# Kernel optimization log

Measured on AMD Instinct MI355X. Metric: run time of the kernel, lower is better.

Reference implementation:

```python
import jax, jax.numpy as jnp
import numpy as np

B, L, D = 2, 2048, 1024
H, E = 16, 64  # n_heads, per-head dim (E_q=E_k=E_v)
EPS = 1e-5


def _layernorm(x):
    # fresh nn.LayerNorm each forward: gamma=1, beta=0, eps=1e-5 (biased var)
    mu = jnp.mean(x, axis=-1, keepdims=True)
    var = jnp.mean(jnp.square(x - mu), axis=-1, keepdims=True)
    return (x - mu) * jax.lax.rsqrt(var + EPS)


def setup_inputs() -> dict:
    key = jax.random.key(0)
    ks = jax.random.split(key, 9)
    s_in = 1.0 / np.sqrt(D)
    s_ctx = 1.0 / np.sqrt(H * E)
    return {
        "query": jax.random.normal(ks[0], (B, L, D), jnp.float32),
        "key": jax.random.normal(ks[1], (B, L, D), jnp.float32),
        "value": jax.random.normal(ks[2], (B, L, D), jnp.float32),
        # torch nn.Linear weights are [out_features, in_features]
        "W_Q": jax.random.uniform(ks[3], (H * E, D), jnp.float32, -s_in, s_in),
        "W_K": jax.random.uniform(ks[4], (H * E, D), jnp.float32, -s_in, s_in),
        "W_V": jax.random.uniform(ks[5], (H * E, D), jnp.float32, -s_in, s_in),
        "W_O": jax.random.uniform(ks[6], (D, H * E), jnp.float32, -s_ctx, s_ctx),
        "fc_w": jax.random.uniform(ks[7], (D, D), jnp.float32, -s_in, s_in),
        "fc_b": jax.random.uniform(ks[8], (D,), jnp.float32, -s_in, s_in),
    }


def reference(query, key, value, W_Q, W_K, W_V, W_O, fc_w, fc_b):
    b = query.shape[0]
    # projections -> [B, H, L, E]
    q = (query @ W_Q.T).reshape(b, -1, H, E).transpose(0, 2, 1, 3)
    k = (key @ W_K.T).reshape(b, -1, H, E).transpose(0, 2, 1, 3)
    v = (value @ W_V.T).reshape(b, -1, H, E).transpose(0, 2, 1, 3)
    scores = jnp.einsum('bhqe,bhke->bhqk', q, k) / np.sqrt(E).astype(np.float32)
    A = jax.nn.softmax(scores, axis=-1)                 # [B,H,Lq,Lk]
    ctx = jnp.einsum('bhqk,bhke->bhqe', A, v)           # [B,H,L,E]
    ctx = ctx.transpose(0, 2, 1, 3).reshape(b, -1, H * E)
    attn_out = ctx @ W_O.T                               # dropout = identity (eval)
    x = _layernorm(attn_out + query)
    out = x @ fc_w.T + fc_b                              # dropout = identity (eval)
    out = _layernorm(x + out)
    return out
```

## Files before the change

kernel.cpp:

```cpp
#include <hip/hip_runtime.h>
#include <stdint.h>

typedef unsigned short u16;
typedef __bf16 bf16x8 __attribute__((ext_vector_type(8)));
typedef __bf16 bf16x4 __attribute__((ext_vector_type(4)));
typedef float f32x4 __attribute__((ext_vector_type(4)));

#define MFMA16(a,b,c) __builtin_amdgcn_mfma_f32_16x16x32_bf16((a),(b),(c),0,0,0)

__device__ __forceinline__ bf16x4 pack4(float a, float b, float c, float d){
  bf16x4 r; r[0]=(__bf16)a; r[1]=(__bf16)b; r[2]=(__bf16)c; r[3]=(__bf16)d; return r;
}

__device__ __forceinline__ void gl2lds16(const void* g, void* l){
  __builtin_amdgcn_global_load_lds(
      (const __attribute__((address_space(1))) unsigned int*)g,
      (__attribute__((address_space(3))) unsigned int*)l, 16, 0, 0);
}

__device__ __forceinline__ bf16x8 ldsfrag(const u16* base, int row, int gr){
  return *(const bf16x8*)(base + row * 64 + ((gr ^ (row & 7)) << 3));
}

template<int NB>
__device__ __forceinline__ void gemm_core(const u16* __restrict__ A,
                                          const u16* __restrict__ Bt,
                                          int N, int K, int mode,
                                          void* __restrict__ Cout,
                                          const float* __restrict__ bias,
                                          float oscale)
{
  __shared__ u16 Al[NB][128 * 64];
  __shared__ u16 Bl[NB][128 * 64];
  const int tid  = threadIdx.x;
  const int lane = tid & 63;
  const int w    = tid >> 6;
  const int wr   = w >> 1, wc = w & 1;
  const int l15  = lane & 15, g = lane >> 4;
  const int rowBase = blockIdx.y << 7;
  const int colBase = blockIdx.x << 7;

  const int srow = tid >> 3;
  const int swz  = ((tid & 7) ^ (srow & 7)) << 3;
  const u16* Ag = A  + (size_t)(rowBase + srow) * K + swz;
  const u16* Bg = Bt + (size_t)(colBase + srow) * K + swz;

  f32x4 acc[4][4];
#pragma unroll
  for (int m = 0; m < 4; ++m)
#pragma unroll
    for (int n = 0; n < 4; ++n) acc[m][n] = f32x4{0.f, 0.f, 0.f, 0.f};

  auto stage = [&](int buf, int k0) {
#pragma unroll
    for (int i = 0; i < 4; ++i) {
      gl2lds16(Ag + (size_t)(i * 32) * K + k0, Al[buf] + i * 2048 + w * 512);
      gl2lds16(Bg + (size_t)(i * 32) * K + k0, Bl[buf] + i * 2048 + w * 512);
    }
  };
  auto compute = [&](int buf) {
    __builtin_amdgcn_s_setprio(1);
#pragma unroll
    for (int kk = 0; kk < 2; ++kk) {
      bf16x8 af[4], bfr[4];
#pragma unroll
      for (int m = 0; m < 4; ++m) af[m]  = ldsfrag(Al[buf], wr * 64 + m * 16 + l15, kk * 4 + g);
#pragma unroll
      for (int n = 0; n < 4; ++n) bfr[n] = ldsfrag(Bl[buf], wc * 64 + n * 16 + l15, kk * 4 + g);
#pragma unroll
      for (int m = 0; m < 4; ++m)
#pragma unroll
        for (int n = 0; n < 4; ++n)
          acc[m][n] = MFMA16(af[m], bfr[n], acc[m][n]);
    }
    __builtin_amdgcn_s_setprio(0);
  };

  if (NB == 2) {
    stage(0, 0);
    __syncthreads();
    int cur = 0;
    for (int k0 = 0; k0 < K; k0 += 64) {
      if (k0 + 64 < K) stage(cur ^ 1, k0 + 64);
      compute(cur);
      __syncthreads();
      cur ^= 1;
    }
  } else {
    for (int k0 = 0; k0 < K; k0 += 64) {
      stage(0, k0);
      __syncthreads();
      compute(0);
      __syncthreads();
    }
  }

#pragma unroll
  for (int m = 0; m < 4; ++m) {
#pragma unroll
    for (int n = 0; n < 4; ++n) {
      const int row0 = rowBase + wr * 64 + m * 16 + g * 4;
      const int col  = colBase + wc * 64 + n * 16 + l15;
      if (mode == 1) {
        const int b = row0 >> 11, l = row0 & 2047;
        const int h = col >> 6,  e = col & 63;
        *(bf16x4*)((u16*)Cout + ((size_t)((((b << 4) + h) << 6) | e) << 11) + l) =
            pack4(acc[m][n][0], acc[m][n][1], acc[m][n][2], acc[m][n][3]);
      } else {
#pragma unroll
        for (int r = 0; r < 4; ++r) {
          const int row = row0 + r;
          const float v = acc[m][n][r];
          if (mode == 0) {
            *(__bf16*)((u16*)Cout + (size_t)row * N + col) = (__bf16)(v * oscale);
          } else if (mode == 2) {
            ((float*)Cout)[(size_t)row * N + col] = v;
          } else {
            ((float*)Cout)[(size_t)row * N + col] = v + bias[col];
          }
        }
      }
    }
  }
}

#define QSCALE 0.18033688011112042f

__global__ __launch_bounds__(256) void k_proj(
    const u16* __restrict__ qb, const u16* __restrict__ kb, const u16* __restrict__ vb,
    const u16* __restrict__ wq, const u16* __restrict__ wk, const u16* __restrict__ wv,
    u16* __restrict__ Qp, u16* __restrict__ Kp, u16* __restrict__ Vt)
{
  const int z = blockIdx.z;
  const u16* A = (z == 0) ? qb : (z == 1) ? kb : vb;
  const u16* B = (z == 0) ? wq : (z == 1) ? wk : wv;
  void* C = (z == 0) ? (void*)Qp : (z == 1) ? (void*)Kp : (void*)Vt;
  gemm_core<1>(A, B, 1024, 1024, (z == 2) ? 1 : 0, C, nullptr, (z == 0) ? QSCALE : 1.0f);
}

__global__ __launch_bounds__(256) void k_gemm_f32(const u16* __restrict__ A,
                                                  const u16* __restrict__ B,
                                                  float* __restrict__ C)
{ gemm_core<2>(A, B, 1024, 1024, 2, (void*)C, nullptr, 1.0f); }

__global__ __launch_bounds__(256) void k_gemm_f32_bias(const u16* __restrict__ A,
                                                       const u16* __restrict__ B,
                                                       float* __restrict__ C,
                                                       const float* __restrict__ bias)
{ gemm_core<2>(A, B, 1024, 1024, 3, (void*)C, bias, 1.0f); }

__global__ __launch_bounds__(256) void k_attn(const u16* __restrict__ Qp,
                                              const u16* __restrict__ Kp,
                                              const u16* __restrict__ Vt,
                                              u16* __restrict__ ctx)
{
  __shared__ u16 Klds[2][64 * 64];
  __shared__ u16 Vlds[2][64 * 64];
  __shared__ u16 Plds[4 * 16 * 64];

  const int tid = threadIdx.x, lane = tid & 63, w = tid >> 6;
  const int l15 = lane & 15, g = lane >> 4, l7 = l15 & 7;
  const int bh = blockIdx.y, b = bh >> 4, h = bh & 15;
  const int q0 = blockIdx.x << 6;

  const u16* Qr = Qp + (((size_t)((b << 11) + q0 + (w << 4) + l15)) << 10) + (h << 6) + (g << 3);
  const bf16x8 bq0 = *(const bf16x8*)(Qr);
  const bf16x8 bq1 = *(const bf16x8*)(Qr + 32);

  f32x4 o[4];
#pragma unroll
  for (int f = 0; f < 4; ++f) o[f] = f32x4{0.f, 0.f, 0.f, 0.f};
  float dsum = 0.f;

  const int srow = tid >> 3;
  const int swz  = ((tid & 7) ^ (srow & 7)) << 3;
  const u16* Kg = Kp + (((size_t)((b << 11) + srow)) << 10) + (h << 6) + swz;
  const u16* Vg = Vt + (((size_t)((bh << 6) + srow)) << 11) + swz;
  u16* Pw = Plds + (w << 10);

  auto stage = [&](int buf, int j0) {
#pragma unroll
    for (int i = 0; i < 2; ++i) {
      gl2lds16(Kg + ((size_t)(j0 + i * 32) << 10), Klds[buf] + i * 2048 + w * 512);
      gl2lds16(Vg + ((size_t)(i * 32) << 11) + j0, Vlds[buf] + i * 2048 + w * 512);
    }
  };

  stage(0, 0);
  __syncthreads();
  int cur = 0;

  for (int j0 = 0; j0 < 2048; j0 += 64) {
    if (j0 + 64 < 2048) stage(cur ^ 1, j0 + 64);

    f32x4 s[4];
#pragma unroll
    for (int f = 0; f < 4; ++f) s[f] = f32x4{0.f, 0.f, 0.f, 0.f};
    __builtin_amdgcn_s_setprio(1);
#pragma unroll
    for (int kk = 0; kk < 2; ++kk) {
      const bf16x8 bq = kk ? bq1 : bq0;
#pragma unroll
      for (int f = 0; f < 4; ++f)
        s[f] = MFMA16(ldsfrag(Klds[cur], f * 16 + l15, kk * 4 + g), bq, s[f]);
    }
    __builtin_amdgcn_s_setprio(0);

#pragma unroll
    for (int f = 0; f < 4; ++f) {
      const float e0 = __builtin_amdgcn_exp2f(s[f][0]);
      const float e1 = __builtin_amdgcn_exp2f(s[f][1]);
      const float e2 = __builtin_amdgcn_exp2f(s[f][2]);
      const float e3 = __builtin_amdgcn_exp2f(s[f][3]);
      dsum += (e0 + e1) + (e2 + e3);
      *(bf16x4*)(Pw + l15 * 64 + ((((2 * f) + (g >> 1)) ^ l7) << 3) + ((g & 1) << 2)) =
          pack4(e0, e1, e2, e3);
    }
    asm volatile("s_waitcnt lgkmcnt(0)" ::: "memory");
    __builtin_amdgcn_sched_barrier(0);

    __builtin_amdgcn_s_setprio(1);
#pragma unroll
    for (int kk = 0; kk < 2; ++kk) {
      const bf16x8 pb = *(const bf16x8*)(Pw + l15 * 64 + (((kk * 4 + g) ^ l7) << 3));
#pragma unroll
      for (int f = 0; f < 4; ++f)
        o[f] = MFMA16(ldsfrag(Vlds[cur], f * 16 + l15, kk * 4 + g), pb, o[f]);
    }
    __builtin_amdgcn_s_setprio(0);
    __syncthreads();
    cur ^= 1;
  }

  dsum += __shfl_xor(dsum, 16, 64);
  dsum += __shfl_xor(dsum, 32, 64);
  const float inv = 1.0f / dsum;
  const size_t rowoff = (((size_t)((b << 11) + q0 + (w << 4) + l15)) << 10) + (h << 6);
#pragma unroll
  for (int f = 0; f < 4; ++f)
    *(bf16x4*)(ctx + rowoff + f * 16 + (g << 2)) =
        pack4(o[f][0] * inv, o[f][1] * inv, o[f][2] * inv, o[f][3] * inv);
}

__global__ __launch_bounds__(256) void k_add_ln(const float* __restrict__ a,
                                                const float* __restrict__ res,
                                                float* __restrict__ xo,
                                                u16* __restrict__ xb)
{
  const int row = blockIdx.x, tid = threadIdx.x;
  const size_t base = (size_t)row << 10;
  float4 t = ((const float4*)(a + base))[tid];
  const float4 rr = ((const float4*)(res + base))[tid];
  t.x += rr.x; t.y += rr.y; t.z += rr.z; t.w += rr.w;
  float s = t.x + t.y + t.z + t.w;
  float q = t.x * t.x + t.y * t.y + t.z * t.z + t.w * t.w;
#pragma unroll
  for (int d = 1; d < 64; d <<= 1) {
    s += __shfl_xor(s, d, 64);
    q += __shfl_xor(q, d, 64);
  }
  __shared__ float ps[4], pq[4];
  const int w = tid >> 6;
  if ((tid & 63) == 0) { ps[w] = s; pq[w] = q; }
  __syncthreads();
  s = ps[0] + ps[1] + ps[2] + ps[3];
  q = pq[0] + pq[1] + pq[2] + pq[3];
  const float mean = s * (1.0f / 1024.0f);
  const float var  = q * (1.0f / 1024.0f) - mean * mean;
  const float inv  = rsqrtf(var + 1e-5f);
  float4 o;
  o.x = (t.x - mean) * inv; o.y = (t.y - mean) * inv;
  o.z = (t.z - mean) * inv; o.w = (t.w - mean) * inv;
  ((float4*)(xo + base))[tid] = o;
  if (xb) {
    ((bf16x4*)(xb + base))[tid] = pack4(o.x, o.y, o.z, o.w);
  }
}

__global__ __launch_bounds__(256) void k_cvt3(const float* __restrict__ q,
                                              const float* __restrict__ k,
                                              const float* __restrict__ v,
                                              u16* __restrict__ qo,
                                              u16* __restrict__ ko,
                                              u16* __restrict__ vo)
{
  const int z = blockIdx.y;
  const float* src = (z == 0) ? q : (z == 1) ? k : v;
  u16* dst = (z == 0) ? qo : (z == 1) ? ko : vo;
  const int i = blockIdx.x * 256 + threadIdx.x;
  const float4 t = ((const float4*)src)[i];
  ((bf16x4*)dst)[i] = pack4(t.x, t.y, t.z, t.w);
}

__global__ __launch_bounds__(256) void k_cvt5(const float* __restrict__ a0,
                                              const float* __restrict__ a1,
                                              const float* __restrict__ a2,
                                              const float* __restrict__ a3,
                                              const float* __restrict__ a4,
                                              u16* __restrict__ o0, u16* __restrict__ o1,
                                              u16* __restrict__ o2, u16* __restrict__ o3,
                                              u16* __restrict__ o4)
{
  const int z = blockIdx.y;
  const float* src = (z == 0) ? a0 : (z == 1) ? a1 : (z == 2) ? a2 : (z == 3) ? a3 : a4;
  u16* dst = (z == 0) ? o0 : (z == 1) ? o1 : (z == 2) ? o2 : (z == 3) ? o3 : o4;
  const int i = blockIdx.x * 256 + threadIdx.x;
  const float4 t = ((const float4*)src)[i];
  ((bf16x4*)dst)[i] = pack4(t.x, t.y, t.z, t.w);
}

extern "C" void kernel_launch(void* const* d_in, const int* in_sizes, int n_in,
                              void* d_out, int out_size, void* d_ws, size_t ws_size,
                              hipStream_t stream)
{
  (void)in_sizes; (void)n_in; (void)out_size; (void)ws_size;
  const float* query = (const float*)d_in[0];
  const float* key   = (const float*)d_in[1];
  const float* value = (const float*)d_in[2];
  const float* W_Q   = (const float*)d_in[3];
  const float* W_K   = (const float*)d_in[4];
  const float* W_V   = (const float*)d_in[5];
  const float* W_O   = (const float*)d_in[6];
  const float* fc_w  = (const float*)d_in[7];
  const float* fc_b  = (const float*)d_in[8];
  float* out = (float*)d_out;
  char* ws = (char*)d_ws;

  u16*   qb   = (u16*)(ws + 0);
  u16*   kb   = (u16*)(ws + 8388608);
  u16*   vb   = (u16*)(ws + 16777216);
  u16*   wq   = (u16*)(ws + 25165824);
  u16*   wk   = (u16*)(ws + 27262976);
  u16*   wv   = (u16*)(ws + 29360128);
  u16*   wo   = (u16*)(ws + 31457280);
  u16*   fw   = (u16*)(ws + 33554432);
  u16*   Qp   = (u16*)(ws + 35651584);
  u16*   Kp   = (u16*)(ws + 44040192);
  u16*   Vt   = (u16*)(ws + 52428800);
  u16*   ctx  = (u16*)(ws + 60817408);
  float* attn = (float*)(ws + 69206016);
  float* x    = (float*)(ws + 85983232);
  u16*   xb   = vb;
  float* y    = (float*)(ws + 0);

  k_cvt3<<<dim3(4096, 3), 256, 0, stream>>>(query, key, value, qb, kb, vb);
  k_cvt5<<<dim3(1024, 5), 256, 0, stream>>>(W_Q, W_K, W_V, W_O, fc_w, wq, wk, wv, wo, fw);
  k_proj<<<dim3(8, 32, 3), 256, 0, stream>>>(qb, kb, vb, wq, wk, wv, Qp, Kp, Vt);
  k_attn<<<dim3(32, 32), 256, 0, stream>>>(Qp, Kp, Vt, ctx);
  k_gemm_f32<<<dim3(8, 32), 256, 0, stream>>>(ctx, wo, attn);
  k_add_ln<<<dim3(4096), 256, 0, stream>>>(attn, query, x, xb);
  k_gemm_f32_bias<<<dim3(8, 32), 256, 0, stream>>>(xb, fw, y, fc_b);
  k_add_ln<<<dim3(4096), 256, 0, stream>>>(y, x, out, nullptr);
}
```

Baseline: 170.6 us.

## Keep K/V fragments in registers, bf16 intermediates, narrower GEMM tiles for O/FC

Attention no longer stages K and V through shared memory with barriers. Each wave loads its K/V MFMA fragments straight from global memory into registers and prefetches the next tile, and the kernel gets an occupancy hint. The output and FC GEMMs use 128x64 tiles for twice as many blocks and write bf16 instead of fp32. The LayerNorm kernels now read bf16 inputs and no longer write the fp32 residual, which reduces memory traffic. In exchange, each wave loads K/V redundantly from global memory, and keeping the residual in bf16 lowers precision.

```diff
diff --git a/kernel.cpp b/kernel.cpp
--- a/kernel.cpp
+++ b/kernel.cpp
@@ -22,7 +22,7 @@
   return *(const bf16x8*)(base + row * 64 + ((gr ^ (row & 7)) << 3));
 }
 
-template<int NB>
+template<int NB, int BN>
 __device__ __forceinline__ void gemm_core(const u16* __restrict__ A,
                                           const u16* __restrict__ Bt,
                                           int N, int K, int mode,
@@ -30,47 +30,49 @@
                                           const float* __restrict__ bias,
                                           float oscale)
 {
+  constexpr int NF = BN / 32;
   __shared__ u16 Al[NB][128 * 64];
-  __shared__ u16 Bl[NB][128 * 64];
+  __shared__ u16 Bl[NB][BN * 64];
   const int tid  = threadIdx.x;
   const int lane = tid & 63;
   const int w    = tid >> 6;
   const int wr   = w >> 1, wc = w & 1;
   const int l15  = lane & 15, g = lane >> 4;
   const int rowBase = blockIdx.y << 7;
-  const int colBase = blockIdx.x << 7;
+  const int colBase = blockIdx.x * BN;
 
   const int srow = tid >> 3;
   const int swz  = ((tid & 7) ^ (srow & 7)) << 3;
   const u16* Ag = A  + (size_t)(rowBase + srow) * K + swz;
   const u16* Bg = Bt + (size_t)(colBase + srow) * K + swz;
 
-  f32x4 acc[4][4];
+  f32x4 acc[4][NF];
 #pragma unroll
   for (int m = 0; m < 4; ++m)
 #pragma unroll
-    for (int n = 0; n < 4; ++n) acc[m][n] = f32x4{0.f, 0.f, 0.f, 0.f};
+    for (int n = 0; n < NF; ++n) acc[m][n] = f32x4{0.f, 0.f, 0.f, 0.f};
 
   auto stage = [&](int buf, int k0) {
 #pragma unroll
-    for (int i = 0; i < 4; ++i) {
+    for (int i = 0; i < 4; ++i)
       gl2lds16(Ag + (size_t)(i * 32) * K + k0, Al[buf] + i * 2048 + w * 512);
+#pragma unroll
+    for (int i = 0; i < BN / 32; ++i)
       gl2lds16(Bg + (size_t)(i * 32) * K + k0, Bl[buf] + i * 2048 + w * 512);
-    }
   };
   auto compute = [&](int buf) {
     __builtin_amdgcn_s_setprio(1);
 #pragma unroll
     for (int kk = 0; kk < 2; ++kk) {
-      bf16x8 af[4], bfr[4];
+      bf16x8 af[4], bfr[NF];
 #pragma unroll
       for (int m = 0; m < 4; ++m) af[m]  = ldsfrag(Al[buf], wr * 64 + m * 16 + l15, kk * 4 + g);
 #pragma unroll
-      for (int n = 0; n < 4; ++n) bfr[n] = ldsfrag(Bl[buf], wc * 64 + n * 16 + l15, kk * 4 + g);
+      for (int n = 0; n < NF; ++n) bfr[n] = ldsfrag(Bl[buf], wc * (BN/2) + n * 16 + l15, kk * 4 + g);
 #pragma unroll
       for (int m = 0; m < 4; ++m)
 #pragma unroll
-        for (int n = 0; n < 4; ++n)
+        for (int n = 0; n < NF; ++n)
           acc[m][n] = MFMA16(af[m], bfr[n], acc[m][n]);
     }
     __builtin_amdgcn_s_setprio(0);
@@ -98,25 +100,24 @@
 #pragma unroll
   for (int m = 0; m < 4; ++m) {
 #pragma unroll
-    for (int n = 0; n < 4; ++n) {
+    for (int n = 0; n < NF; ++n) {
       const int row0 = rowBase + wr * 64 + m * 16 + g * 4;
-      const int col  = colBase + wc * 64 + n * 16 + l15;
+      const int col  = colBase + wc * (BN/2) + n * 16 + l15;
       if (mode == 1) {
         const int b = row0 >> 11, l = row0 & 2047;
         const int h = col >> 6,  e = col & 63;
         *(bf16x4*)((u16*)Cout + ((size_t)((((b << 4) + h) << 6) | e) << 11) + l) =
             pack4(acc[m][n][0], acc[m][n][1], acc[m][n][2], acc[m][n][3]);
       } else {
+        const float bb = (mode == 4) ? bias[col] : 0.f;
 #pragma unroll
         for (int r = 0; r < 4; ++r) {
           const int row = row0 + r;
           const float v = acc[m][n][r];
           if (mode == 0) {
             *(__bf16*)((u16*)Cout + (size_t)row * N + col) = (__bf16)(v * oscale);
-          } else if (mode == 2) {
-            ((float*)Cout)[(size_t)row * N + col] = v;
           } else {
-            ((float*)Cout)[(size_t)row * N + col] = v + bias[col];
+            *(__bf16*)((u16*)Cout + (size_t)row * N + col) = (__bf16)(v + bb);
           }
         }
       }
@@ -135,27 +136,25 @@
   const u16* A = (z == 0) ? qb : (z == 1) ? kb : vb;
   const u16* B = (z == 0) ? wq : (z == 1) ? wk : wv;
   void* C = (z == 0) ? (void*)Qp : (z == 1) ? (void*)Kp : (void*)Vt;
-  gemm_core<1>(A, B, 1024, 1024, (z == 2) ? 1 : 0, C, nullptr, (z == 0) ? QSCALE : 1.0f);
-}
-
-__global__ __launch_bounds__(256) void k_gemm_f32(const u16* __restrict__ A,
-                                                  const u16* __restrict__ B,
-                                                  float* __restrict__ C)
-{ gemm_core<2>(A, B, 1024, 1024, 2, (void*)C, nullptr, 1.0f); }
-
-__global__ __launch_bounds__(256) void k_gemm_f32_bias(const u16* __restrict__ A,
-                                                       const u16* __restrict__ B,
-                                                       float* __restrict__ C,
-                                                       const float* __restrict__ bias)
-{ gemm_core<2>(A, B, 1024, 1024, 3, (void*)C, bias, 1.0f); }
-
-__global__ __launch_bounds__(256) void k_attn(const u16* __restrict__ Qp,
-                                              const u16* __restrict__ Kp,
-                                              const u16* __restrict__ Vt,
-                                              u16* __restrict__ ctx)
-{
-  __shared__ u16 Klds[2][64 * 64];
-  __shared__ u16 Vlds[2][64 * 64];
+  gemm_core<1, 128>(A, B, 1024, 1024, (z == 2) ? 1 : 0, C, nullptr, (z == 0) ? QSCALE : 1.0f);
+}
+
+__global__ __launch_bounds__(256) void k_gemm_o(const u16* __restrict__ A,
+                                                const u16* __restrict__ B,
+                                                u16* __restrict__ C)
+{ gemm_core<2, 64>(A, B, 1024, 1024, 0, (void*)C, nullptr, 1.0f); }
+
+__global__ __launch_bounds__(256) void k_gemm_fc(const u16* __restrict__ A,
+                                                 const u16* __restrict__ B,
+                                                 u16* __restrict__ C,
+                                                 const float* __restrict__ bias)
+{ gemm_core<2, 64>(A, B, 1024, 1024, 4, (void*)C, bias, 1.0f); }
+
+__global__ __launch_bounds__(256, 3) void k_attn(const u16* __restrict__ Qp,
+                                                 const u16* __restrict__ Kp,
+                                                 const u16* __restrict__ Vt,
+                                                 u16* __restrict__ ctx)
+{
   __shared__ u16 Plds[4 * 16 * 64];
 
   const int tid = threadIdx.x, lane = tid & 63, w = tid >> 6;
@@ -167,44 +166,45 @@
   const bf16x8 bq0 = *(const bf16x8*)(Qr);
   const bf16x8 bq1 = *(const bf16x8*)(Qr + 32);
 
+  const f32x4 zero4 = {0.f, 0.f, 0.f, 0.f};
   f32x4 o[4];
 #pragma unroll
-  for (int f = 0; f < 4; ++f) o[f] = f32x4{0.f, 0.f, 0.f, 0.f};
+  for (int f = 0; f < 4; ++f) o[f] = zero4;
   float dsum = 0.f;
 
-  const int srow = tid >> 3;
-  const int swz  = ((tid & 7) ^ (srow & 7)) << 3;
-  const u16* Kg = Kp + (((size_t)((b << 11) + srow)) << 10) + (h << 6) + swz;
-  const u16* Vg = Vt + (((size_t)((bh << 6) + srow)) << 11) + swz;
+  const u16* Kbase = Kp + (((size_t)(b << 11)) << 10) + (h << 6);
+  const u16* Vbase = Vt + (((size_t)(bh << 6)) << 11);
+
+  bf16x8 kf[4][2], vf[4][2];
+#pragma unroll
+  for (int f = 0; f < 4; ++f)
+#pragma unroll
+    for (int kk = 0; kk < 2; ++kk) {
+      kf[f][kk] = *(const bf16x8*)(Kbase + ((size_t)(f * 16 + l15) << 10) + kk * 32 + (g << 3));
+      vf[f][kk] = *(const bf16x8*)(Vbase + ((size_t)(f * 16 + l15) << 11) + kk * 32 + (g << 3));
+    }
+
   u16* Pw = Plds + (w << 10);
 
-  auto stage = [&](int buf, int j0) {
-#pragma unroll
-    for (int i = 0; i < 2; ++i) {
-      gl2lds16(Kg + ((size_t)(j0 + i * 32) << 10), Klds[buf] + i * 2048 + w * 512);
-      gl2lds16(Vg + ((size_t)(i * 32) << 11) + j0, Vlds[buf] + i * 2048 + w * 512);
-    }
-  };
-
-  stage(0, 0);
-  __syncthreads();
-  int cur = 0;
-
   for (int j0 = 0; j0 < 2048; j0 += 64) {
-    if (j0 + 64 < 2048) stage(cur ^ 1, j0 + 64);
+    const int jn = j0 + 64;
 
     f32x4 s[4];
-#pragma unroll
-    for (int f = 0; f < 4; ++f) s[f] = f32x4{0.f, 0.f, 0.f, 0.f};
     __builtin_amdgcn_s_setprio(1);
 #pragma unroll
-    for (int kk = 0; kk < 2; ++kk) {
-      const bf16x8 bq = kk ? bq1 : bq0;
+    for (int f = 0; f < 4; ++f) {
+      s[f] = MFMA16(kf[f][0], bq0, zero4);
+      s[f] = MFMA16(kf[f][1], bq1, s[f]);
+    }
+    __builtin_amdgcn_s_setprio(0);
+
+    if (jn < 2048) {
 #pragma unroll
       for (int f = 0; f < 4; ++f)
-        s[f] = MFMA16(ldsfrag(Klds[cur], f * 16 + l15, kk * 4 + g), bq, s[f]);
-    }
-    __builtin_amdgcn_s_setprio(0);
+#pragma unroll
+        for (int kk = 0; kk < 2; ++kk)
+          kf[f][kk] = *(const bf16x8*)(Kbase + ((size_t)(jn + f * 16 + l15) << 10) + kk * 32 + (g << 3));
+    }
 
 #pragma unroll
     for (int f = 0; f < 4; ++f) {
@@ -225,11 +225,17 @@
       const bf16x8 pb = *(const bf16x8*)(Pw + l15 * 64 + (((kk * 4 + g) ^ l7) << 3));
 #pragma unroll
       for (int f = 0; f < 4; ++f)
-        o[f] = MFMA16(ldsfrag(Vlds[cur], f * 16 + l15, kk * 4 + g), pb, o[f]);
+        o[f] = MFMA16(vf[f][kk], pb, o[f]);
     }
     __builtin_amdgcn_s_setprio(0);
-    __syncthreads();
-    cur ^= 1;
+
+    if (jn < 2048) {
+#pragma unroll
+      for (int f = 0; f < 4; ++f)
+#pragma unroll
+        for (int kk = 0; kk < 2; ++kk)
+          vf[f][kk] = *(const bf16x8*)(Vbase + ((size_t)(f * 16 + l15) << 11) + jn + kk * 32 + (g << 3));
+    }
   }
 
   dsum += __shfl_xor(dsum, 16, 64);
@@ -242,16 +248,7 @@
         pack4(o[f][0] * inv, o[f][1] * inv, o[f][2] * inv, o[f][3] * inv);
 }
 
-__global__ __launch_bounds__(256) void k_add_ln(const float* __restrict__ a,
-                                                const float* __restrict__ res,
-                                                float* __restrict__ xo,
-                                                u16* __restrict__ xb)
-{
-  const int row = blockIdx.x, tid = threadIdx.x;
-  const size_t base = (size_t)row << 10;
-  float4 t = ((const float4*)(a + base))[tid];
-  const float4 rr = ((const float4*)(res + base))[tid];
-  t.x += rr.x; t.y += rr.y; t.z += rr.z; t.w += rr.w;
+__device__ __forceinline__ void ln_stats(float4 t, int tid, float& mean, float& inv){
   float s = t.x + t.y + t.z + t.w;
   float q = t.x * t.x + t.y * t.y + t.z * t.z + t.w * t.w;
 #pragma unroll
@@ -265,16 +262,45 @@
   __syncthreads();
   s = ps[0] + ps[1] + ps[2] + ps[3];
   q = pq[0] + pq[1] + pq[2] + pq[3];
-  const float mean = s * (1.0f / 1024.0f);
-  const float var  = q * (1.0f / 1024.0f) - mean * mean;
-  const float inv  = rsqrtf(var + 1e-5f);
+  mean = s * (1.0f / 1024.0f);
+  const float var = q * (1.0f / 1024.0f) - mean * mean;
+  inv = rsqrtf(var + 1e-5f);
+}
+
+__global__ __launch_bounds__(256) void k_ln1(const u16* __restrict__ a,
+                                             const float* __restrict__ res,
+                                             u16* __restrict__ xb)
+{
+  const int row = blockIdx.x, tid = threadIdx.x;
+  const size_t base = (size_t)row << 10;
+  const bf16x4 av = ((const bf16x4*)(a + base))[tid];
+  const float4 rr = ((const float4*)(res + base))[tid];
+  float4 t;
+  t.x = (float)av[0] + rr.x; t.y = (float)av[1] + rr.y;
+  t.z = (float)av[2] + rr.z; t.w = (float)av[3] + rr.w;
+  float mean, inv;
+  ln_stats(t, tid, mean, inv);
+  ((bf16x4*)(xb + base))[tid] = pack4((t.x - mean) * inv, (t.y - mean) * inv,
+                                      (t.z - mean) * inv, (t.w - mean) * inv);
+}
+
+__global__ __launch_bounds__(256) void k_ln2(const u16* __restrict__ a,
+                                             const u16* __restrict__ res,
+                                             float* __restrict__ out)
+{
+  const int row = blockIdx.x, tid = threadIdx.x;
+  const size_t base = (size_t)row << 10;
+  const bf16x4 av = ((const bf16x4*)(a + base))[tid];
+  const bf16x4 rv = ((const bf16x4*)(res + base))[tid];
+  float4 t;
+  t.x = (float)av[0] + (float)rv[0]; t.y = (float)av[1] + (float)rv[1];
+  t.z = (float)av[2] + (float)rv[2]; t.w = (float)av[3] + (float)rv[3];
+  float mean, inv;
+  ln_stats(t, tid, mean, inv);
   float4 o;
   o.x = (t.x - mean) * inv; o.y = (t.y - mean) * inv;
   o.z = (t.z - mean) * inv; o.w = (t.w - mean) * inv;
-  ((float4*)(xo + base))[tid] = o;
-  if (xb) {
-    ((bf16x4*)(xb + base))[tid] = pack4(o.x, o.y, o.z, o.w);
-  }
+  ((float4*)(out + base))[tid] = o;
 }
 
 __global__ __launch_bounds__(256) void k_cvt3(const float* __restrict__ q,
@@ -326,29 +352,28 @@
   float* out = (float*)d_out;
   char* ws = (char*)d_ws;
 
-  u16*   qb   = (u16*)(ws + 0);
-  u16*   kb   = (u16*)(ws + 8388608);
-  u16*   vb   = (u16*)(ws + 16777216);
-  u16*   wq   = (u16*)(ws + 25165824);
-  u16*   wk   = (u16*)(ws + 27262976);
-  u16*   wv   = (u16*)(ws + 29360128);
-  u16*   wo   = (u16*)(ws + 31457280);
-  u16*   fw   = (u16*)(ws + 33554432);
-  u16*   Qp   = (u16*)(ws + 35651584);
-  u16*   Kp   = (u16*)(ws + 44040192);
-  u16*   Vt   = (u16*)(ws + 52428800);
-  u16*   ctx  = (u16*)(ws + 60817408);
-  float* attn = (float*)(ws + 69206016);
-  float* x    = (float*)(ws + 85983232);
-  u16*   xb   = vb;
-  float* y    = (float*)(ws + 0);
+  u16*   qb    = (u16*)(ws + 0);
+  u16*   kb    = (u16*)(ws + 8388608);
+  u16*   vb    = (u16*)(ws + 16777216);
+  u16*   wq    = (u16*)(ws + 25165824);
+  u16*   wk    = (u16*)(ws + 27262976);
+  u16*   wv    = (u16*)(ws + 29360128);
+  u16*   wo    = (u16*)(ws + 31457280);
+  u16*   fw    = (u16*)(ws + 33554432);
+  u16*   Qp    = (u16*)(ws + 35651584);
+  u16*   Kp    = (u16*)(ws + 44040192);
+  u16*   Vt    = (u16*)(ws + 52428800);
+  u16*   ctx   = (u16*)(ws + 60817408);
+  u16*   attnb = (u16*)(ws + 69206016);
+  u16*   xb    = vb;
+  u16*   yb    = qb;
 
   k_cvt3<<<dim3(4096, 3), 256, 0, stream>>>(query, key, value, qb, kb, vb);
   k_cvt5<<<dim3(1024, 5), 256, 0, stream>>>(W_Q, W_K, W_V, W_O, fc_w, wq, wk, wv, wo, fw);
   k_proj<<<dim3(8, 32, 3), 256, 0, stream>>>(qb, kb, vb, wq, wk, wv, Qp, Kp, Vt);
   k_attn<<<dim3(32, 32), 256, 0, stream>>>(Qp, Kp, Vt, ctx);
-  k_gemm_f32<<<dim3(8, 32), 256, 0, stream>>>(ctx, wo, attn);
-  k_add_ln<<<dim3(4096), 256, 0, stream>>>(attn, query, x, xb);
-  k_gemm_f32_bias<<<dim3(8, 32), 256, 0, stream>>>(xb, fw, y, fc_b);
-  k_add_ln<<<dim3(4096), 256, 0, stream>>>(y, x, out, nullptr);
-}
+  k_gemm_o<<<dim3(16, 32), 256, 0, stream>>>(ctx, wo, attnb);
+  k_ln1<<<dim3(4096), 256, 0, stream>>>(attnb, query, xb);
+  k_gemm_fc<<<dim3(16, 32), 256, 0, stream>>>(xb, fw, yb, fc_b);
+  k_ln2<<<dim3(4096), 256, 0, stream>>>(yb, xb, out);
+}
```

Result: slower. 326.4 us (+91.3%).
